# Kernel tuning notes

Hardware: AMD Instinct MI355X
Metric: run time of the kernel (lower is better)

The kernel has to match this reference:

```python
import jax, jax.numpy as jnp
import numpy as np

ALPHA = 0.2  # LeakyReLU slope


def _gat_scores(Wh, a_src, a_dst):
    # Wh: (..., N, H); score[i, j] = a_src . Wh_i + a_dst . Wh_j
    s_src = jnp.einsum('...nh,...h->...n', Wh, a_src)
    s_dst = jnp.einsum('...nh,...h->...n', Wh, a_dst)
    e = jax.nn.leaky_relu(s_src[..., :, None] + s_dst[..., None, :], ALPHA)
    # adj is all-ones -> mask is a no-op; softmax over neighbors j
    return jax.nn.softmax(e, axis=-1)


def setup_inputs() -> dict:
    key = jax.random.key(0)
    ks = jax.random.split(key, 9)
    B, S, F = 32, 12, 128
    H, K, C, N = 64, 8, 64, 512

    def xavier(k, shape, gain=1.414):
        fan_in, fan_out = shape[-2], shape[-1]
        lim = gain * np.sqrt(6.0 / (fan_in + fan_out))
        return jax.random.uniform(k, shape, jnp.float32, -lim, lim)

    x = jax.random.normal(ks[0], (B, S, F), jnp.float32)
    W_heads = xavier(ks[1], (K, F, H))
    a_heads = xavier(ks[2], (K, 2 * H, 1))[..., 0]  # (K, 2H)
    a1_heads, a2_heads = a_heads[:, :H], a_heads[:, H:]
    W_out = xavier(ks[3], (K * H, C))
    a_out = xavier(ks[4], (2 * C, 1))[:, 0]
    a1_out, a2_out = a_out[:C], a_out[C:]
    lim = 1.0 / np.sqrt(N * C)
    Wf = jax.random.uniform(ks[5], (C, N * C), jnp.float32, -lim, lim)
    bf = jax.random.uniform(ks[6], (C,), jnp.float32, -lim, lim)
    return {"x": x, "W_heads": W_heads, "a1_heads": a1_heads,
            "a2_heads": a2_heads, "W_out": W_out, "a1_out": a1_out,
            "a2_out": a2_out, "Wf": Wf, "bf": bf}


def reference(x, W_heads, a1_heads, a2_heads, W_out, a1_out, a2_out, Wf, bf):
    N = 512
    B = x.shape[0]
    h = jnp.broadcast_to(x[:, -1, None, :], (B, N, x.shape[-1]))  # (B, N, F)

    # Multi-head GAT, heads vectorized: Wh (B, K, N, H)
    Wh = jnp.einsum('bnf,kfh->bknh', h, W_heads)
    att = _gat_scores(Wh, a1_heads, a2_heads)            # (B, K, N, N)
    hp = jnp.einsum('bkij,bkjh->bkih', att, Wh)           # (B, K, N, H)
    hp = jax.nn.elu(hp)
    B_, K, N_, H = hp.shape
    h_cat = hp.transpose(0, 2, 1, 3).reshape(B_, N_, K * H)  # concat heads

    # Output GAT layer (concat=False -> no ELU)
    Wh_o = jnp.einsum('bnf,fc->bnc', h_cat, W_out)        # (B, N, C)
    att_o = _gat_scores(Wh_o, a1_out, a2_out)             # (B, N, N)
    out = jnp.einsum('bij,bjc->bic', att_o, Wh_o)         # (B, N, C)

    out = out.reshape(B, -1)
    return out @ Wf.T + bf
```

## Files before the change

kernel.cpp:

```cpp
#include <hip/hip_runtime.h>
#include <hip/hip_bf16.h>


__global__ __launch_bounds__(256) void kA(const float* __restrict__ Wf,
                                          const float* __restrict__ x,
                                          const float* __restrict__ W_heads,
                                          float* __restrict__ ws) {
    float* wsumT = ws;
    float* HP    = ws + 4096;
    const int t = threadIdx.x;

    if (blockIdx.x < 64) {
        const int c = blockIdx.x;
        const float* row = Wf + (size_t)c * 32768;
        const int p = t & 15;
        const int ng = t >> 4;
        float ax = 0.f, ay = 0.f, az = 0.f, aw = 0.f;
#pragma unroll 8
        for (int i = 0; i < 32; ++i) {
            const float4 v = *reinterpret_cast<const float4*>(row + (ng + 16 * i) * 64 + p * 4);
            ax += v.x; ay += v.y; az += v.z; aw += v.w;
        }
        __shared__ float s[16][64];
        s[ng][p * 4 + 0] = ax; s[ng][p * 4 + 1] = ay;
        s[ng][p * 4 + 2] = az; s[ng][p * 4 + 3] = aw;
        __syncthreads();
        if (t < 64) {
            float sum = 0.f;
#pragma unroll
            for (int g = 0; g < 16; ++g) sum += s[g][t];
            wsumT[t * 64 + c] = sum;
        }
    } else {
        const int idx = blockIdx.x - 64;
        const int k  = idx >> 4;
        const int hq = (idx & 15) * 4;
        __shared__ float xl[32][129];
#pragma unroll
        for (int r = 0; r < 4; ++r) {
            const int id = t + 256 * r;
            const int b = id >> 5, fq = id & 31;
            const float4 v = *reinterpret_cast<const float4*>(x + b * 1536 + 1408 + fq * 4);
            xl[b][fq * 4 + 0] = v.x; xl[b][fq * 4 + 1] = v.y;
            xl[b][fq * 4 + 2] = v.z; xl[b][fq * 4 + 3] = v.w;
        }
        __syncthreads();
        const int fh = t & 1;
        const int e  = (t >> 1) & 3;
        const int b  = t >> 3;
        const float* wp = W_heads + k * 8192 + fh * 4096 + hq + e;
        float acc = 0.f;
#pragma unroll 16
        for (int f = 0; f < 64; ++f)
            acc += xl[b][fh * 64 + f] * wp[f * 64];
        acc += __shfl_xor(acc, 1);
        if (fh == 0) {
            const float v = (acc > 0.f) ? acc : expm1f(acc);
            HP[b * 512 + k * 64 + hq + e] = v;
        }
    }
}

__global__ __launch_bounds__(256) void kB(const float* __restrict__ W_out,
                                          const float* __restrict__ bias,
                                          const float* __restrict__ ws,
                                          float* __restrict__ out) {
    const float* wsumT = ws;
    const float* HP    = ws + 4096;
    const int b = blockIdx.x;
    const int t = threadIdx.x;

    __shared__ float hp[512];
    __shared__ float s[16][64];
    __shared__ float who[64];
    __shared__ float red[256];

    hp[t]       = HP[b * 512 + t];
    hp[t + 256] = HP[b * 512 + 256 + t];
    __syncthreads();

    {
        const int cq = t & 15;
        const int jg = t >> 4;
        float ax = 0.f, ay = 0.f, az = 0.f, aw = 0.f;
#pragma unroll 8
        for (int i = 0; i < 32; ++i) {
            const int j = jg + 16 * i;
            const float4 w = *reinterpret_cast<const float4*>(W_out + j * 64 + cq * 4);
            const float h = hp[j];
            ax += h * w.x; ay += h * w.y; az += h * w.z; aw += h * w.w;
        }
        s[jg][cq * 4 + 0] = ax; s[jg][cq * 4 + 1] = ay;
        s[jg][cq * 4 + 2] = az; s[jg][cq * 4 + 3] = aw;
    }
    __syncthreads();
    if (t < 64) {
        float sum = 0.f;
#pragma unroll
        for (int g = 0; g < 16; ++g) sum += s[g][t];
        who[t] = sum;
    }
    __syncthreads();

    {
        const int c  = t & 63;
        const int cg = t >> 6;
        float acc = 0.f;
#pragma unroll
        for (int c2 = cg * 16; c2 < cg * 16 + 16; ++c2)
            acc += who[c2] * wsumT[c2 * 64 + c];
        red[t] = acc;
    }
    __syncthreads();
    if (t < 64)
        out[b * 64 + t] = red[t] + red[t + 64] + red[t + 128] + red[t + 192] + bias[t];
}

extern "C" void kernel_launch(void* const* d_in, const int* in_sizes, int n_in,
                              void* d_out, int out_size, void* d_ws, size_t ws_size,
                              hipStream_t stream) {
    const float* x       = (const float*)d_in[0];
    const float* W_heads = (const float*)d_in[1];
    const float* W_out   = (const float*)d_in[4];
    const float* Wf      = (const float*)d_in[7];
    const float* bias    = (const float*)d_in[8];
    float* ws = (float*)d_ws;

    kA<<<192, 256, 0, stream>>>(Wf, x, W_heads, ws);
    kB<<<32, 256, 0, stream>>>(W_out, bias, ws, (float*)d_out);
}
```

Before: 81.46 us.

## Fuse head and output stages into one kernel with atomic-flag grid sync

Merges the two kernels into one launch. 32 blocks compute per-batch hidden features and the W_out projection, publish them to workspace and bump an atomic counter. 64 blocks compute the Wf row sums, then spin-wait on the counter and produce the final outputs. This removes a kernel boundary and reorganises the head projection per batch, but it relies on all blocks being co-resident and adds a memset launch to reset the flag.

```diff
diff --git a/kernel.cpp b/kernel.cpp
--- a/kernel.cpp
+++ b/kernel.cpp
@@ -1,19 +1,83 @@
 #include <hip/hip_runtime.h>
-#include <hip/hip_bf16.h>
 
 
-__global__ __launch_bounds__(256) void kA(const float* __restrict__ Wf,
-                                          const float* __restrict__ x,
-                                          const float* __restrict__ W_heads,
-                                          float* __restrict__ ws) {
-    float* wsumT = ws;
-    float* HP    = ws + 4096;
+__global__ __launch_bounds__(256) void kFused(const float* __restrict__ Wf,
+                                              const float* __restrict__ x,
+                                              const float* __restrict__ W_heads,
+                                              const float* __restrict__ W_out,
+                                              const float* __restrict__ bias,
+                                              float* __restrict__ ws,
+                                              float* __restrict__ out) {
+    float* whoG = ws;
+    unsigned int* flag = (unsigned int*)(ws + 2048);
     const int t = threadIdx.x;
 
-    if (blockIdx.x < 64) {
-        const int c = blockIdx.x;
+    __shared__ float s[16][64];
+    __shared__ float xl[128];
+    __shared__ float hp[512];
+    __shared__ float rs[64];
+
+    if (blockIdx.x < 32) {
+        const int b = blockIdx.x;
+        if (t < 32) {
+            const float4 v = *reinterpret_cast<const float4*>(x + b * 1536 + 1408 + t * 4);
+            xl[t * 4 + 0] = v.x; xl[t * 4 + 1] = v.y;
+            xl[t * 4 + 2] = v.z; xl[t * 4 + 3] = v.w;
+        }
+        __syncthreads();
+        {
+            const int fh = t & 1;
+            const int q  = t >> 1;
+            const int k  = q >> 4;
+            const int hq = (q & 15) * 4;
+            const float* wp = W_heads + k * 8192 + fh * 4096 + hq;
+            float a0 = 0.f, a1 = 0.f, a2 = 0.f, a3 = 0.f;
+#pragma unroll 8
+            for (int f = 0; f < 64; ++f) {
+                const float4 w = *reinterpret_cast<const float4*>(wp + f * 64);
+                const float xv = xl[fh * 64 + f];
+                a0 += xv * w.x; a1 += xv * w.y; a2 += xv * w.z; a3 += xv * w.w;
+            }
+            a0 += __shfl_xor(a0, 1); a1 += __shfl_xor(a1, 1);
+            a2 += __shfl_xor(a2, 1); a3 += __shfl_xor(a3, 1);
+            if (fh == 0) {
+                const int j = k * 64 + hq;
+                hp[j + 0] = (a0 > 0.f) ? a0 : expm1f(a0);
+                hp[j + 1] = (a1 > 0.f) ? a1 : expm1f(a1);
+                hp[j + 2] = (a2 > 0.f) ? a2 : expm1f(a2);
+                hp[j + 3] = (a3 > 0.f) ? a3 : expm1f(a3);
+            }
+        }
+        __syncthreads();
+        {
+            const int cq = t & 15;
+            const int jg = t >> 4;
+            float ax = 0.f, ay = 0.f, az = 0.f, aw = 0.f;
+#pragma unroll 8
+            for (int i = 0; i < 32; ++i) {
+                const int j = jg + 16 * i;
+                const float4 w = *reinterpret_cast<const float4*>(W_out + j * 64 + cq * 4);
+                const float h = hp[j];
+                ax += h * w.x; ay += h * w.y; az += h * w.z; aw += h * w.w;
+            }
+            s[jg][cq * 4 + 0] = ax; s[jg][cq * 4 + 1] = ay;
+            s[jg][cq * 4 + 2] = az; s[jg][cq * 4 + 3] = aw;
+        }
+        __syncthreads();
+        if (t < 64) {
+            float sum = 0.f;
+#pragma unroll
+            for (int g = 0; g < 16; ++g) sum += s[g][t];
+            whoG[b * 64 + t] = sum;
+        }
+        __threadfence();
+        __syncthreads();
+        if (t == 0)
+            __hip_atomic_fetch_add(flag, 1u, __ATOMIC_RELEASE, __HIP_MEMORY_SCOPE_AGENT);
+    } else {
+        const int c = blockIdx.x - 32;
         const float* row = Wf + (size_t)c * 32768;
-        const int p = t & 15;
+        const int p  = t & 15;
         const int ng = t >> 4;
         float ax = 0.f, ay = 0.f, az = 0.f, aw = 0.f;
 #pragma unroll 8
@@ -21,7 +85,6 @@
             const float4 v = *reinterpret_cast<const float4*>(row + (ng + 16 * i) * 64 + p * 4);
             ax += v.x; ay += v.y; az += v.z; aw += v.w;
         }
-        __shared__ float s[16][64];
         s[ng][p * 4 + 0] = ax; s[ng][p * 4 + 1] = ay;
         s[ng][p * 4 + 2] = az; s[ng][p * 4 + 3] = aw;
         __syncthreads();
@@ -29,91 +92,22 @@
             float sum = 0.f;
 #pragma unroll
             for (int g = 0; g < 16; ++g) sum += s[g][t];
-            wsumT[t * 64 + c] = sum;
-        }
-    } else {
-        const int idx = blockIdx.x - 64;
-        const int k  = idx >> 4;
-        const int hq = (idx & 15) * 4;
-        __shared__ float xl[32][129];
-#pragma unroll
-        for (int r = 0; r < 4; ++r) {
-            const int id = t + 256 * r;
-            const int b = id >> 5, fq = id & 31;
-            const float4 v = *reinterpret_cast<const float4*>(x + b * 1536 + 1408 + fq * 4);
-            xl[b][fq * 4 + 0] = v.x; xl[b][fq * 4 + 1] = v.y;
-            xl[b][fq * 4 + 2] = v.z; xl[b][fq * 4 + 3] = v.w;
+            rs[t] = sum;
         }
         __syncthreads();
-        const int fh = t & 1;
-        const int e  = (t >> 1) & 3;
-        const int b  = t >> 3;
-        const float* wp = W_heads + k * 8192 + fh * 4096 + hq + e;
-        float acc = 0.f;
-#pragma unroll 16
-        for (int f = 0; f < 64; ++f)
-            acc += xl[b][fh * 64 + f] * wp[f * 64];
-        acc += __shfl_xor(acc, 1);
-        if (fh == 0) {
-            const float v = (acc > 0.f) ? acc : expm1f(acc);
-            HP[b * 512 + k * 64 + hq + e] = v;
-        }
-    }
-}
-
-__global__ __launch_bounds__(256) void kB(const float* __restrict__ W_out,
-                                          const float* __restrict__ bias,
-                                          const float* __restrict__ ws,
-                                          float* __restrict__ out) {
-    const float* wsumT = ws;
-    const float* HP    = ws + 4096;
-    const int b = blockIdx.x;
-    const int t = threadIdx.x;
-
-    __shared__ float hp[512];
-    __shared__ float s[16][64];
-    __shared__ float who[64];
-    __shared__ float red[256];
-
-    hp[t]       = HP[b * 512 + t];
-    hp[t + 256] = HP[b * 512 + 256 + t];
-    __syncthreads();
-
-    {
-        const int cq = t & 15;
-        const int jg = t >> 4;
-        float ax = 0.f, ay = 0.f, az = 0.f, aw = 0.f;
-#pragma unroll 8
-        for (int i = 0; i < 32; ++i) {
-            const int j = jg + 16 * i;
-            const float4 w = *reinterpret_cast<const float4*>(W_out + j * 64 + cq * 4);
-            const float h = hp[j];
-            ax += h * w.x; ay += h * w.y; az += h * w.z; aw += h * w.w;
-        }
-        s[jg][cq * 4 + 0] = ax; s[jg][cq * 4 + 1] = ay;
-        s[jg][cq * 4 + 2] = az; s[jg][cq * 4 + 3] = aw;
-    }
-    __syncthreads();
-    if (t < 64) {
-        float sum = 0.f;
-#pragma unroll
-        for (int g = 0; g < 16; ++g) sum += s[g][t];
-        who[t] = sum;
-    }
-    __syncthreads();
-
-    {
-        const int c  = t & 63;
-        const int cg = t >> 6;
+        while (__hip_atomic_load(flag, __ATOMIC_ACQUIRE, __HIP_MEMORY_SCOPE_AGENT) < 32u)
+            __builtin_amdgcn_s_sleep(2);
+        const int b = t >> 3;
+        const int g = t & 7;
         float acc = 0.f;
 #pragma unroll
-        for (int c2 = cg * 16; c2 < cg * 16 + 16; ++c2)
-            acc += who[c2] * wsumT[c2 * 64 + c];
-        red[t] = acc;
+        for (int c2 = g * 8; c2 < g * 8 + 8; ++c2)
+            acc += whoG[b * 64 + c2] * rs[c2];
+        acc += __shfl_xor(acc, 1);
+        acc += __shfl_xor(acc, 2);
+        acc += __shfl_xor(acc, 4);
+        if (g == 0) out[b * 64 + c] = acc + bias[c];
     }
-    __syncthreads();
-    if (t < 64)
-        out[b * 64 + t] = red[t] + red[t + 64] + red[t + 128] + red[t + 192] + bias[t];
 }
 
 extern "C" void kernel_launch(void* const* d_in, const int* in_sizes, int n_in,
@@ -126,6 +120,6 @@
     const float* bias    = (const float*)d_in[8];
     float* ws = (float*)d_ws;
 
-    kA<<<192, 256, 0, stream>>>(Wf, x, W_heads, ws);
-    kB<<<32, 256, 0, stream>>>(W_out, bias, ws, (float*)d_out);
+    hipMemsetAsync((char*)d_ws + 8192, 0, 4, stream);
+    kFused<<<96, 256, 0, stream>>>(Wf, x, W_heads, W_out, bias, ws, (float*)d_out);
 }
```

Result: slower. 96.79 us (+18.8%).
